# Kernel tuning notes

Measured on AMD Instinct MI355X. Metric: run time of the kernel, lower is better.

## Reference

```python
import jax, jax.numpy as jnp
import numpy as np

NUM_EXPERTS = 4
TOP_K = 2


def setup_inputs() -> dict:
    key = jax.random.key(0)
    ks = jax.random.split(key, 16)
    B, L, D, E, H = 8, 768, 1024, NUM_EXPERTS, 4096
    s = 0.02
    return {
        "context_c": jax.random.normal(ks[0], (B, L, D), jnp.float32),
        "time_cond": jax.random.normal(ks[1], (B, D), jnp.float32),
        "gate_w": jax.random.normal(ks[2], (3 * D, E), jnp.float32) * s,
        "gate_b": jnp.zeros((E,), jnp.float32),
        "time_w": jax.random.normal(ks[3], (D, 2 * E), jnp.float32) * s,
        "time_b": jnp.zeros((2 * E,), jnp.float32),
        "ew1": jax.random.normal(ks[4], (E, D, H), jnp.float32) * s,
        "eb1": jnp.zeros((E, H), jnp.float32),
        "ew2": jax.random.normal(ks[5], (E, H, D), jnp.float32) * s,
        "eb2": jnp.zeros((E, D), jnp.float32),
        "sw1": jax.random.normal(ks[6], (D, H), jnp.float32) * s,
        "sb1": jnp.zeros((H,), jnp.float32),
        "sw2": jax.random.normal(ks[7], (H, D), jnp.float32) * s,
        "sb2": jnp.zeros((D,), jnp.float32),
    }


def reference(context_c, time_cond, gate_w, gate_b, time_w, time_b,
              ew1, eb1, ew2, eb2, sw1, sb1, sw2, sb2):
    B, L, D = context_c.shape
    E, K = NUM_EXPERTS, TOP_K
    L_head = L_wrist = L // 3

    head = context_c[:, :L_head]                       # (B, Lh, D)
    wrist = context_c[:, L_head:L_head + L_wrist]      # (B, Lw, D)
    proprio = context_c[:, L_head + L_wrist:]          # (B, Lp, D)

    # modality-combination aggregates for the gate
    full_agg = context_c.mean(axis=1)
    hp_agg = jnp.concatenate([head, proprio], axis=1).mean(axis=1)
    wp_agg = jnp.concatenate([wrist, proprio], axis=1).mean(axis=1)
    gate_in = jnp.concatenate([full_agg, hp_agg, wp_agg], axis=-1)  # (B, 3D)

    gate_logits = gate_in @ gate_w + gate_b            # (B, E)
    mod = jax.nn.silu(time_cond) @ time_w + time_b     # (B, 2E)
    scale, shift = jnp.split(mod, 2, axis=-1)
    gate_logits = gate_logits * (1.0 + scale) + shift

    gate_scores = jax.nn.softmax(gate_logits, axis=-1)
    topk_w, topk_i = jax.lax.top_k(gate_scores, K)     # (B, K)
    topk_w = topk_w / (topk_w.sum(axis=-1, keepdims=True) + 1e-8)

    # per-sample combine weight per expert: (B, E)
    onehot = (topk_i[..., None] == jnp.arange(E)[None, None, :]).astype(context_c.dtype)
    w_be = jnp.sum(topk_w[..., None] * onehot, axis=1)

    # modality token masks per expert: expert 1 skips wrist, expert 2 skips head
    mask = np.ones((E, L), dtype=np.float32)
    mask[1, L_head:L_head + L_wrist] = 0.0
    mask[2, :L_head] = 0.0
    mask = jnp.asarray(mask)

    out = jnp.zeros_like(context_c)
    for e in range(E):  # small fixed expert loop; FFN is tokenwise so masking == routing
        h = jax.nn.gelu(context_c @ ew1[e] + eb1[e], approximate=True)
        y = h @ ew2[e] + eb2[e]                        # (B, L, D)
        out = out + (w_be[:, e][:, None, None] * mask[e][None, :, None]) * y

    shared = jax.nn.gelu(context_c @ sw1 + sb1, approximate=True) @ sw2 + sb2
    return out + shared
```

## Files before the change

### kernel.cpp

```cpp
#include <hip/hip_runtime.h>

using bf16x8 = __attribute__((ext_vector_type(8))) short;
using f32x4  = __attribute__((ext_vector_type(4))) float;
using u16x4  = __attribute__((ext_vector_type(4))) unsigned short;

#define AS1(p) ((__attribute__((address_space(1))) void*)(p))
#define AS3(p) ((__attribute__((address_space(3))) void*)(p))

__device__ __forceinline__ unsigned short f2bf(float f){
  unsigned int x = __float_as_uint(f);
  unsigned int r = (x + 0x7FFFu + ((x >> 16) & 1u)) >> 16;
  return (unsigned short)r;
}
__device__ __forceinline__ float gelu_tanh(float x){
  float u = 0.7978845608028654f * (x + 0.044715f * x * x * x);
  float t = 1.f - 2.f / (__expf(2.f * u) + 1.f);
  return 0.5f * x * (1.f + t);
}

static constexpr int BB = 8, LL = 768, DD = 1024, HH = 4096, TT = 6144;

__global__ __launch_bounds__(256) void k0_transpose(const float* __restrict__ srcE,
                                                    const float* __restrict__ srcS,
                                                    unsigned short* __restrict__ dst,
                                                    int R, int C){
  __shared__ float tile[64][65];
  int z = blockIdx.z;
  const float* src = (z < 4) ? srcE + (size_t)z * R * C : srcS;
  unsigned short* d = dst + (size_t)z * R * C;
  int c0 = blockIdx.x * 64, r0 = blockIdx.y * 64;
  int tx = threadIdx.x & 15, ty = threadIdx.x >> 4;
  #pragma unroll
  for (int rep = 0; rep < 4; rep++){
    int r = ty + rep * 16;
    float4 v = *(const float4*)(src + (size_t)(r0 + r) * C + c0 + tx * 4);
    tile[r][tx * 4 + 0] = v.x; tile[r][tx * 4 + 1] = v.y;
    tile[r][tx * 4 + 2] = v.z; tile[r][tx * 4 + 3] = v.w;
  }
  __syncthreads();
  #pragma unroll
  for (int rep = 0; rep < 4; rep++){
    int c = ty + rep * 16;
    u16x4 o;
    o[0] = f2bf(tile[tx * 4 + 0][c]); o[1] = f2bf(tile[tx * 4 + 1][c]);
    o[2] = f2bf(tile[tx * 4 + 2][c]); o[3] = f2bf(tile[tx * 4 + 3][c]);
    *(u16x4*)(d + (size_t)(c0 + c) * R + r0 + tx * 4) = o;
  }
}

__global__ __launch_bounds__(256) void k1x_cvt_partial(const float* __restrict__ X,
                                                       unsigned short* __restrict__ Xb,
                                                       float* __restrict__ part){
  int ch = blockIdx.x, b = blockIdx.y, t = threadIdx.x;
  size_t rowbase = ((size_t)(b * LL + ch * 32)) * DD;
  const float4* src = (const float4*)(X + rowbase);
  u16x4* dst = (u16x4*)(Xb + rowbase);
  float4 s; s.x = s.y = s.z = s.w = 0.f;
  for (int l = 0; l < 32; l++){
    float4 v = src[l * 256 + t];
    u16x4 o;
    o[0] = f2bf(v.x); o[1] = f2bf(v.y); o[2] = f2bf(v.z); o[3] = f2bf(v.w);
    dst[l * 256 + t] = o;
    s.x += v.x; s.y += v.y; s.z += v.z; s.w += v.w;
  }
  ((float4*)(part + ((size_t)(b * 24 + ch)) * DD))[t] = s;
}

__global__ __launch_bounds__(256) void k1b_gate(const float* __restrict__ part,
                                                const float* __restrict__ tc,
                                                const float* __restrict__ gw,
                                                const float* __restrict__ gb,
                                                const float* __restrict__ tw,
                                                const float* __restrict__ tb,
                                                float* __restrict__ wtop, int* __restrict__ itop){
  int b = blockIdx.x, t = threadIdx.x;
  __shared__ float glog[4], gmod[8];
  if (t < 4) glog[t] = 0.f;
  if (t < 8) gmod[t] = 0.f;
  __syncthreads();
  float lacc[4] = {0.f,0.f,0.f,0.f};
  float macc[8] = {0.f,0.f,0.f,0.f,0.f,0.f,0.f,0.f};
  for (int dd = 0; dd < 4; dd++){
    int d = dd * 256 + t;
    const float* pb = part + (size_t)b * 24 * DD + d;
    float sh = 0.f, sw = 0.f, sp = 0.f;
    for (int c2 = 0; c2 < 8; c2++){
      sh += pb[(0  + c2) * DD];
      sw += pb[(8  + c2) * DD];
      sp += pb[(16 + c2) * DD];
    }
    float fa = (sh + sw + sp) * (1.f / 768.f);
    float hp = (sh + sp) * (1.f / 512.f);
    float wp = (sw + sp) * (1.f / 512.f);
    #pragma unroll
    for (int e = 0; e < 4; e++){
      lacc[e] += fa * gw[(size_t)d * 4 + e]
               + hp * gw[(size_t)(DD + d) * 4 + e]
               + wp * gw[(size_t)(2 * DD + d) * 4 + e];
    }
    float v = tc[(size_t)b * DD + d];
    float sl = v / (1.f + __expf(-v));
    #pragma unroll
    for (int j = 0; j < 8; j++) macc[j] += sl * tw[(size_t)d * 8 + j];
  }
  #pragma unroll
  for (int e = 0; e < 4; e++) atomicAdd(&glog[e], lacc[e]);
  #pragma unroll
  for (int j = 0; j < 8; j++) atomicAdd(&gmod[j], macc[j]);
  __syncthreads();
  if (t == 0){
    float lg[4];
    #pragma unroll
    for (int e = 0; e < 4; e++){
      float sc = gmod[e]     + tb[e];
      float sf = gmod[4 + e] + tb[4 + e];
      lg[e] = (glog[e] + gb[e]) * (1.f + sc) + sf;
    }
    float mx = fmaxf(fmaxf(lg[0], lg[1]), fmaxf(lg[2], lg[3]));
    float p[4], s = 0.f;
    #pragma unroll
    for (int e = 0; e < 4; e++){ p[e] = __expf(lg[e] - mx); s += p[e]; }
    #pragma unroll
    for (int e = 0; e < 4; e++) p[e] /= s;
    int i0 = 0;
    for (int e = 1; e < 4; e++) if (p[e] > p[i0]) i0 = e;
    int i1 = (i0 == 0) ? 1 : 0;
    for (int e = 0; e < 4; e++) if (e != i0 && p[e] > p[i1]) i1 = e;
    float den = p[i0] + p[i1] + 1e-8f;
    wtop[b * 2 + 0] = p[i0] / den;  wtop[b * 2 + 1] = p[i1] / den;
    itop[b * 2 + 0] = i0;           itop[b * 2 + 1] = i1;
  }
}

__device__ __forceinline__ void gemm_core(const unsigned short* __restrict__ A,
                                          const unsigned short* __restrict__ B,
                                          size_t lda, size_t ldb, int nkt,
                                          unsigned short* ldsA, unsigned short* ldsB,
                                          f32x4 (&acc)[4][4]){
  int tid = threadIdx.x;
  int lane = tid & 63, wave = tid >> 6;
  int quad = lane >> 4, r = lane & 15;
  int wm = (wave >> 1) * 64, wn = (wave & 1) * 64;
  int wavebase = tid & 192;
  for (int kt = 0; kt < nkt; kt++){
    int k0 = kt * 64;
    #pragma unroll
    for (int i = 0; i < 4; i++){
      int g = i * 256 + tid;
      int m = g >> 3, slot = g & 7;
      int c = slot ^ (m & 7);
      const unsigned short* gpA = A + (size_t)m * lda + (k0 + c * 8);
      const unsigned short* gpB = B + (size_t)m * ldb + (k0 + c * 8);
      unsigned short* lp = ldsA + (size_t)(i * 256 + wavebase) * 8;
      __builtin_amdgcn_global_load_lds(AS1(gpA), AS3(lp), 16, 0, 0);
      unsigned short* lq = ldsB + (size_t)(i * 256 + wavebase) * 8;
      __builtin_amdgcn_global_load_lds(AS1(gpB), AS3(lq), 16, 0, 0);
    }
    __syncthreads();
    #pragma unroll
    for (int ks = 0; ks < 2; ks++){
      int cc = ks * 4 + quad;
      bf16x8 af[4], bfv[4];
      #pragma unroll
      for (int t2 = 0; t2 < 4; t2++){
        int m = wm + t2 * 16 + r;
        af[t2] = *(const bf16x8*)(ldsA + ((size_t)m * 8 + (cc ^ (m & 7))) * 8);
        int n = wn + t2 * 16 + r;
        bfv[t2] = *(const bf16x8*)(ldsB + ((size_t)n * 8 + (cc ^ (n & 7))) * 8);
      }
      #pragma unroll
      for (int mi = 0; mi < 4; mi++)
        #pragma unroll
        for (int ni = 0; ni < 4; ni++)
          acc[mi][ni] = __builtin_amdgcn_mfma_f32_16x16x32_bf16(af[mi], bfv[ni], acc[mi][ni], 0, 0, 0);
    }
    __syncthreads();
  }
}

__device__ __forceinline__ void mask_weight(int e, int seg, float& w){
  if ((e == 1 && seg == 1) || (e == 2 && seg == 0)) w = 0.f;
}

__global__ __launch_bounds__(256) void k2_gemm1(const unsigned short* __restrict__ Xb,
                                                const unsigned short* __restrict__ w1t,
                                                const float* __restrict__ eb1,
                                                const float* __restrict__ sb1,
                                                const float* __restrict__ wtop,
                                                const int* __restrict__ itop,
                                                unsigned short* __restrict__ Hws){
  int m0 = blockIdx.x * 128, n0 = blockIdx.y * 128, slot = blockIdx.z;
  int b = m0 / LL, seg = (m0 % LL) / 256;
  int mat; float w;
  if (slot == 0){ mat = 4; w = 1.f; }
  else {
    int k = slot - 1;
    mat = itop[b * 2 + k];
    w = wtop[b * 2 + k];
    mask_weight(mat, seg, w);
    if (w == 0.f) return;
  }
  __shared__ __align__(16) unsigned short ldsA[128 * 64];
  __shared__ __align__(16) unsigned short ldsB[128 * 64];
  f32x4 acc[4][4];
  #pragma unroll
  for (int mi = 0; mi < 4; mi++)
    #pragma unroll
    for (int ni = 0; ni < 4; ni++)
      #pragma unroll
      for (int c = 0; c < 4; c++) acc[mi][ni][c] = 0.f;

  const unsigned short* Abase = Xb + (size_t)m0 * DD;
  const unsigned short* Bbase = w1t + (size_t)mat * HH * DD + (size_t)n0 * DD;
  gemm_core(Abase, Bbase, DD, DD, DD / 64, ldsA, ldsB, acc);

  int tid = threadIdx.x, lane = tid & 63, wave = tid >> 6;
  int quad = lane >> 4, r = lane & 15;
  int wm = (wave >> 1) * 64, wn = (wave & 1) * 64;
  const float* b1 = (mat == 4) ? sb1 : eb1 + (size_t)mat * HH;
  unsigned short* Hout = Hws + (size_t)slot * TT * HH;
  #pragma unroll
  for (int ni = 0; ni < 4; ni++){
    int col = n0 + wn + ni * 16 + r;
    float bias = b1[col];
    #pragma unroll
    for (int mi = 0; mi < 4; mi++){
      #pragma unroll
      for (int r2 = 0; r2 < 4; r2++){
        int row = m0 + wm + mi * 16 + quad * 4 + r2;
        float v = gelu_tanh(acc[mi][ni][r2] + bias) * w;
        Hout[(size_t)row * HH + col] = f2bf(v);
      }
    }
  }
}

__global__ __launch_bounds__(256) void k3a_gemm2(const unsigned short* __restrict__ Hws,
                                                 const unsigned short* __restrict__ w2t,
                                                 const float* __restrict__ eb2,
                                                 const float* __restrict__ sb2,
                                                 const float* __restrict__ wtop,
                                                 const int* __restrict__ itop,
                                                 float* __restrict__ out,
                                                 float* __restrict__ p1){
  int m0 = blockIdx.x * 128, n0 = blockIdx.y * 128, kh = blockIdx.z;
  int b = m0 / LL, seg = (m0 % LL) / 256;
  __shared__ __align__(16) unsigned short ldsA[128 * 64];
  __shared__ __align__(16) unsigned short ldsB[128 * 64];
  f32x4 acc[4][4];
  #pragma unroll
  for (int mi = 0; mi < 4; mi++)
    #pragma unroll
    for (int ni = 0; ni < 4; ni++)
      #pragma unroll
      for (int c = 0; c < 4; c++) acc[mi][ni][c] = 0.f;

  int emat[2]; float ew[2];
  #pragma unroll
  for (int k = 0; k < 2; k++){
    emat[k] = itop[b * 2 + k];
    ew[k] = wtop[b * 2 + k];
    mask_weight(emat[k], seg, ew[k]);
  }
  for (int slot = 0; slot < 3; slot++){
    int mat;
    if (slot == 0) mat = 4;
    else { if (ew[slot - 1] == 0.f) continue; mat = emat[slot - 1]; }
    const unsigned short* Abase = Hws + (size_t)slot * TT * HH + (size_t)m0 * HH + kh * 2048;
    const unsigned short* Bbase = w2t + (size_t)mat * DD * HH + (size_t)n0 * HH + kh * 2048;
    gemm_core(Abase, Bbase, HH, HH, 2048 / 64, ldsA, ldsB, acc);
  }
  int tid = threadIdx.x, lane = tid & 63, wave = tid >> 6;
  int quad = lane >> 4, r = lane & 15;
  int wm = (wave >> 1) * 64, wn = (wave & 1) * 64;
  if (kh == 0){
    #pragma unroll
    for (int ni = 0; ni < 4; ni++){
      int col = n0 + wn + ni * 16 + r;
      float bias = sb2[col];
      if (ew[0] > 0.f) bias += ew[0] * eb2[(size_t)emat[0] * DD + col];
      if (ew[1] > 0.f) bias += ew[1] * eb2[(size_t)emat[1] * DD + col];
      #pragma unroll
      for (int mi = 0; mi < 4; mi++)
        #pragma unroll
        for (int r2 = 0; r2 < 4; r2++){
          int row = m0 + wm + mi * 16 + quad * 4 + r2;
          out[(size_t)row * DD + col] = acc[mi][ni][r2] + bias;
        }
    }
  } else {
    #pragma unroll
    for (int ni = 0; ni < 4; ni++){
      int col = n0 + wn + ni * 16 + r;
      #pragma unroll
      for (int mi = 0; mi < 4; mi++)
        #pragma unroll
        for (int r2 = 0; r2 < 4; r2++){
          int row = m0 + wm + mi * 16 + quad * 4 + r2;
          p1[(size_t)row * DD + col] = acc[mi][ni][r2];
        }
    }
  }
}

__global__ __launch_bounds__(256) void k3r_reduce(float* __restrict__ out,
                                                  const float* __restrict__ p1){
  size_t i = (size_t)blockIdx.x * 256 + threadIdx.x;
  float4 a = ((const float4*)out)[i];
  float4 b = ((const float4*)p1)[i];
  a.x += b.x; a.y += b.y; a.z += b.z; a.w += b.w;
  ((float4*)out)[i] = a;
}

extern "C" void kernel_launch(void* const* d_in, const int* in_sizes, int n_in,
                              void* d_out, int out_size, void* d_ws, size_t ws_size,
                              hipStream_t stream){
  const float* X   = (const float*)d_in[0];
  const float* tc  = (const float*)d_in[1];
  const float* gw  = (const float*)d_in[2];
  const float* gb  = (const float*)d_in[3];
  const float* tw  = (const float*)d_in[4];
  const float* tb  = (const float*)d_in[5];
  const float* ew1 = (const float*)d_in[6];
  const float* eb1 = (const float*)d_in[7];
  const float* ew2 = (const float*)d_in[8];
  const float* eb2 = (const float*)d_in[9];
  const float* sw1 = (const float*)d_in[10];
  const float* sb1 = (const float*)d_in[11];
  const float* sw2 = (const float*)d_in[12];
  const float* sb2 = (const float*)d_in[13];
  float* out = (float*)d_out;
  char* ws = (char*)d_ws;

  const size_t off_part = 0;
  const size_t off_wtop = 786432;
  const size_t off_itop = 786560;
  const size_t off_xb   = 1ull << 20;
  const size_t off_w1t  = 14ull << 20;
  const size_t off_w2t  = off_w1t + 41943040ull;
  const size_t off_h    = off_w2t + 41943040ull;
  const size_t need     = off_h + 150994944ull;
  if (ws_size < need) return;

  float* part = (float*)(ws + off_part);
  float* wtop = (float*)(ws + off_wtop);
  int*   itop = (int*)(ws + off_itop);
  unsigned short* Xb  = (unsigned short*)(ws + off_xb);
  unsigned short* w1t = (unsigned short*)(ws + off_w1t);
  unsigned short* w2t = (unsigned short*)(ws + off_w2t);
  unsigned short* Hws = (unsigned short*)(ws + off_h);
  float* p1 = (float*)(ws + off_w1t);

  k1x_cvt_partial<<<dim3(24, 8), 256, 0, stream>>>(X, Xb, part);
  k0_transpose<<<dim3(64, 16, 5), 256, 0, stream>>>(ew1, sw1, w1t, 1024, 4096);
  k0_transpose<<<dim3(16, 64, 5), 256, 0, stream>>>(ew2, sw2, w2t, 4096, 1024);
  k1b_gate<<<dim3(8), 256, 0, stream>>>(part, tc, gw, gb, tw, tb, wtop, itop);
  k2_gemm1<<<dim3(48, 32, 3), 256, 0, stream>>>(Xb, w1t, eb1, sb1, wtop, itop, Hws);
  k3a_gemm2<<<dim3(48, 8, 2), 256, 0, stream>>>(Hws, w2t, eb2, sb2, wtop, itop, out, p1);
  k3r_reduce<<<dim3(6144), 256, 0, stream>>>(out, p1);
}
```

Baseline: 712.2 us.

## Switch GEMMs to 256x256 tiles with 8 waves and double-buffered LDS pipeline

Replaces the 128x128, 4-wave GEMM core with a 256x256 tile computed by 8 waves. LDS is double-buffered, and global-to-LDS prefetches for later K steps are interleaved between quarter-tile MFMA phases, using explicit barriers, waitcnt and setprio. The goal is more data reuse per byte loaded and hiding global load latency behind MFMA work. The cost is a much larger LDS footprint (128KB per block) and fewer blocks in the k3a_gemm2 grid (192 instead of 768), which may underfill the GPU.

```diff
diff --git a/kernel.cpp b/kernel.cpp
--- a/kernel.cpp
+++ b/kernel.cpp
@@ -132,49 +132,117 @@
   }
 }
 
-__device__ __forceinline__ void gemm_core(const unsigned short* __restrict__ A,
-                                          const unsigned short* __restrict__ B,
-                                          size_t lda, size_t ldb, int nkt,
-                                          unsigned short* ldsA, unsigned short* ldsB,
-                                          f32x4 (&acc)[4][4]){
-  int tid = threadIdx.x;
-  int lane = tid & 63, wave = tid >> 6;
-  int quad = lane >> 4, r = lane & 15;
-  int wm = (wave >> 1) * 64, wn = (wave & 1) * 64;
-  int wavebase = tid & 192;
+#define MMA_Q(AF, BQ, MH, NH)                                                   \
+  {                                                                             \
+    _Pragma("unroll") for (int ks = 0; ks < 2; ks++)                            \
+    _Pragma("unroll") for (int mf = 0; mf < 4; mf++)                            \
+    _Pragma("unroll") for (int nf = 0; nf < 2; nf++)                            \
+      acc[(MH)*4+mf][(NH)*2+nf] = __builtin_amdgcn_mfma_f32_16x16x32_bf16(      \
+          (AF)[mf][ks], (BQ)[nf][ks], acc[(MH)*4+mf][(NH)*2+nf], 0, 0, 0);      \
+  }
+
+__device__ __forceinline__ void gemm256_core(const unsigned short* __restrict__ A,
+                                             const unsigned short* __restrict__ B,
+                                             int lda, int ldb, int nkt,
+                                             unsigned short* ldsA,
+                                             unsigned short* ldsB,
+                                             f32x4 (&acc)[8][4]){
+  const int t = threadIdx.x;
+  const int lane = t & 63, quad = lane >> 4, r = lane & 15;
+  const int wave = t >> 6, wm = wave >> 2, wn = wave & 3;
+  const int welem = (t & 448) * 8;
+
+  int offA[2], offB[2];
+  #pragma unroll
+  for (int j = 0; j < 2; j++){
+    int x = t * 16 + j * 8192;
+    int y = x ^ (((x >> 9) & 1) << 5);
+    int cr = y >> 7, kel = (y & 127) >> 1;
+    offA[j] = (((cr >> 6) << 7) + (cr & 63)) * lda + kel;
+    offB[j] = (((cr >> 5) << 6) + (cr & 31)) * ldb + kel;
+  }
+  const int ldam = 64 * lda, ldbn = 32 * ldb;
+
+  auto stA = [&](int buf, int mh, int kt){
+    #pragma unroll
+    for (int j = 0; j < 2; j++)
+      __builtin_amdgcn_global_load_lds(AS1(A + offA[j] + mh * ldam + kt * 64),
+          AS3(ldsA + (buf * 2 + mh) * 8192 + welem + j * 4096), 16, 0, 0);
+  };
+  auto stB = [&](int buf, int nh, int kt){
+    #pragma unroll
+    for (int j = 0; j < 2; j++)
+      __builtin_amdgcn_global_load_lds(AS1(B + offB[j] + nh * ldbn + kt * 64),
+          AS3(ldsB + (buf * 2 + nh) * 8192 + welem + j * 4096), 16, 0, 0);
+  };
+  auto ldA = [&](int buf, int mh, bf16x8 (&dst)[4][2]){
+    #pragma unroll
+    for (int mf = 0; mf < 4; mf++){
+      int cr = wm * 64 + mf * 16 + r;
+      const unsigned short* p = ldsA + (buf * 2 + mh) * 8192 + cr * 64;
+      int sw = (cr & 4) ? 16 : 0;
+      dst[mf][0] = *(const bf16x8*)(p + ((quad * 8) ^ sw));
+      dst[mf][1] = *(const bf16x8*)(p + 32 + ((quad * 8) ^ sw));
+    }
+  };
+  auto ldB = [&](int buf, int nh, bf16x8 (&dst)[2][2]){
+    #pragma unroll
+    for (int nf = 0; nf < 2; nf++){
+      int cc = wn * 32 + nf * 16 + r;
+      const unsigned short* p = ldsB + (buf * 2 + nh) * 8192 + cc * 64;
+      int sw = (cc & 4) ? 16 : 0;
+      dst[nf][0] = *(const bf16x8*)(p + ((quad * 8) ^ sw));
+      dst[nf][1] = *(const bf16x8*)(p + 32 + ((quad * 8) ^ sw));
+    }
+  };
+
+  stA(0, 0, 0); stB(0, 0, 0); stB(0, 1, 0); stA(0, 1, 0);
+  stA(1, 0, 1); stB(1, 0, 1); stB(1, 1, 1);
+  asm volatile("s_waitcnt vmcnt(6)" ::: "memory");
+  __builtin_amdgcn_s_barrier();
+
+  bf16x8 af[4][2], b0[2][2], b1[2][2];
   for (int kt = 0; kt < nkt; kt++){
-    int k0 = kt * 64;
-    #pragma unroll
-    for (int i = 0; i < 4; i++){
-      int g = i * 256 + tid;
-      int m = g >> 3, slot = g & 7;
-      int c = slot ^ (m & 7);
-      const unsigned short* gpA = A + (size_t)m * lda + (k0 + c * 8);
-      const unsigned short* gpB = B + (size_t)m * ldb + (k0 + c * 8);
-      unsigned short* lp = ldsA + (size_t)(i * 256 + wavebase) * 8;
-      __builtin_amdgcn_global_load_lds(AS1(gpA), AS3(lp), 16, 0, 0);
-      unsigned short* lq = ldsB + (size_t)(i * 256 + wavebase) * 8;
-      __builtin_amdgcn_global_load_lds(AS1(gpB), AS3(lq), 16, 0, 0);
-    }
-    __syncthreads();
-    #pragma unroll
-    for (int ks = 0; ks < 2; ks++){
-      int cc = ks * 4 + quad;
-      bf16x8 af[4], bfv[4];
-      #pragma unroll
-      for (int t2 = 0; t2 < 4; t2++){
-        int m = wm + t2 * 16 + r;
-        af[t2] = *(const bf16x8*)(ldsA + ((size_t)m * 8 + (cc ^ (m & 7))) * 8);
-        int n = wn + t2 * 16 + r;
-        bfv[t2] = *(const bf16x8*)(ldsB + ((size_t)n * 8 + (cc ^ (n & 7))) * 8);
-      }
-      #pragma unroll
-      for (int mi = 0; mi < 4; mi++)
-        #pragma unroll
-        for (int ni = 0; ni < 4; ni++)
-          acc[mi][ni] = __builtin_amdgcn_mfma_f32_16x16x32_bf16(af[mi], bfv[ni], acc[mi][ni], 0, 0, 0);
-    }
-    __syncthreads();
+    int buf = kt & 1;
+    bool pf1 = (kt + 1 < nkt), pf2 = (kt + 2 < nkt);
+    ldA(buf, 0, af); ldB(buf, 0, b0);
+    if (pf1) stA(buf ^ 1, 1, kt + 1);
+    __builtin_amdgcn_s_barrier();
+    asm volatile("s_waitcnt lgkmcnt(0)" ::: "memory");
+    __builtin_amdgcn_sched_barrier(0);
+    __builtin_amdgcn_s_setprio(1);
+    MMA_Q(af, b0, 0, 0);
+    __builtin_amdgcn_s_setprio(0);
+    __builtin_amdgcn_s_barrier();
+    ldB(buf, 1, b1);
+    if (pf2) stA(buf, 0, kt + 2);
+    __builtin_amdgcn_s_barrier();
+    asm volatile("s_waitcnt lgkmcnt(0)" ::: "memory");
+    __builtin_amdgcn_sched_barrier(0);
+    __builtin_amdgcn_s_setprio(1);
+    MMA_Q(af, b1, 0, 1);
+    __builtin_amdgcn_s_setprio(0);
+    __builtin_amdgcn_s_barrier();
+    ldA(buf, 1, af);
+    if (pf2) stB(buf, 0, kt + 2);
+    __builtin_amdgcn_s_barrier();
+    asm volatile("s_waitcnt lgkmcnt(0)" ::: "memory");
+    __builtin_amdgcn_sched_barrier(0);
+    __builtin_amdgcn_s_setprio(1);
+    MMA_Q(af, b1, 1, 1);
+    __builtin_amdgcn_s_setprio(0);
+    __builtin_amdgcn_s_barrier();
+    if (pf2) stB(buf, 1, kt + 2);
+    __builtin_amdgcn_s_barrier();
+    __builtin_amdgcn_sched_barrier(0);
+    __builtin_amdgcn_s_setprio(1);
+    MMA_Q(af, b0, 1, 0);
+    __builtin_amdgcn_s_setprio(0);
+    if (pf1){
+      if (pf2) asm volatile("s_waitcnt vmcnt(6)" ::: "memory");
+      else     asm volatile("s_waitcnt vmcnt(0)" ::: "memory");
+    }
+    __builtin_amdgcn_s_barrier();
   }
 }
 
@@ -182,14 +250,14 @@
   if ((e == 1 && seg == 1) || (e == 2 && seg == 0)) w = 0.f;
 }
 
-__global__ __launch_bounds__(256) void k2_gemm1(const unsigned short* __restrict__ Xb,
-                                                const unsigned short* __restrict__ w1t,
-                                                const float* __restrict__ eb1,
-                                                const float* __restrict__ sb1,
-                                                const float* __restrict__ wtop,
-                                                const int* __restrict__ itop,
-                                                unsigned short* __restrict__ Hws){
-  int m0 = blockIdx.x * 128, n0 = blockIdx.y * 128, slot = blockIdx.z;
+__global__ __launch_bounds__(512, 2) void k2_gemm1(const unsigned short* __restrict__ Xb,
+                                                   const unsigned short* __restrict__ w1t,
+                                                   const float* __restrict__ eb1,
+                                                   const float* __restrict__ sb1,
+                                                   const float* __restrict__ wtop,
+                                                   const int* __restrict__ itop,
+                                                   unsigned short* __restrict__ Hws){
+  int m0 = blockIdx.x * 256, n0 = blockIdx.y * 256, slot = blockIdx.z;
   int b = m0 / LL, seg = (m0 % LL) / 256;
   int mat; float w;
   if (slot == 0){ mat = 4; w = 1.f; }
@@ -200,56 +268,54 @@
     mask_weight(mat, seg, w);
     if (w == 0.f) return;
   }
-  __shared__ __align__(16) unsigned short ldsA[128 * 64];
-  __shared__ __align__(16) unsigned short ldsB[128 * 64];
-  f32x4 acc[4][4];
-  #pragma unroll
-  for (int mi = 0; mi < 4; mi++)
+  __shared__ __align__(16) unsigned short ldsA[32768];
+  __shared__ __align__(16) unsigned short ldsB[32768];
+  f32x4 acc[8][4];
+  #pragma unroll
+  for (int mi = 0; mi < 8; mi++)
     #pragma unroll
     for (int ni = 0; ni < 4; ni++)
       #pragma unroll
       for (int c = 0; c < 4; c++) acc[mi][ni][c] = 0.f;
 
-  const unsigned short* Abase = Xb + (size_t)m0 * DD;
-  const unsigned short* Bbase = w1t + (size_t)mat * HH * DD + (size_t)n0 * DD;
-  gemm_core(Abase, Bbase, DD, DD, DD / 64, ldsA, ldsB, acc);
-
-  int tid = threadIdx.x, lane = tid & 63, wave = tid >> 6;
-  int quad = lane >> 4, r = lane & 15;
-  int wm = (wave >> 1) * 64, wn = (wave & 1) * 64;
+  gemm256_core(Xb + (size_t)m0 * DD,
+               w1t + (size_t)mat * HH * DD + (size_t)n0 * DD,
+               DD, DD, DD / 64, ldsA, ldsB, acc);
+
+  int t = threadIdx.x, lane = t & 63, wave = t >> 6;
+  int quad = lane >> 4, r = lane & 15, wm = wave >> 2, wn = wave & 3;
   const float* b1 = (mat == 4) ? sb1 : eb1 + (size_t)mat * HH;
   unsigned short* Hout = Hws + (size_t)slot * TT * HH;
   #pragma unroll
   for (int ni = 0; ni < 4; ni++){
-    int col = n0 + wn + ni * 16 + r;
+    int col = n0 + wn * 64 + ni * 16 + r;
     float bias = b1[col];
     #pragma unroll
-    for (int mi = 0; mi < 4; mi++){
+    for (int mi = 0; mi < 8; mi++){
       #pragma unroll
       for (int r2 = 0; r2 < 4; r2++){
-        int row = m0 + wm + mi * 16 + quad * 4 + r2;
-        float v = gelu_tanh(acc[mi][ni][r2] + bias) * w;
-        Hout[(size_t)row * HH + col] = f2bf(v);
+        int row = m0 + wm * 128 + mi * 16 + quad * 4 + r2;
+        Hout[(size_t)row * HH + col] = f2bf(gelu_tanh(acc[mi][ni][r2] + bias) * w);
       }
     }
   }
 }
 
-__global__ __launch_bounds__(256) void k3a_gemm2(const unsigned short* __restrict__ Hws,
-                                                 const unsigned short* __restrict__ w2t,
-                                                 const float* __restrict__ eb2,
-                                                 const float* __restrict__ sb2,
-                                                 const float* __restrict__ wtop,
-                                                 const int* __restrict__ itop,
-                                                 float* __restrict__ out,
-                                                 float* __restrict__ p1){
-  int m0 = blockIdx.x * 128, n0 = blockIdx.y * 128, kh = blockIdx.z;
+__global__ __launch_bounds__(512, 2) void k3a_gemm2(const unsigned short* __restrict__ Hws,
+                                                    const unsigned short* __restrict__ w2t,
+                                                    const float* __restrict__ eb2,
+                                                    const float* __restrict__ sb2,
+                                                    const float* __restrict__ wtop,
+                                                    const int* __restrict__ itop,
+                                                    float* __restrict__ out,
+                                                    float* __restrict__ p1){
+  int m0 = blockIdx.x * 256, n0 = blockIdx.y * 256, kh = blockIdx.z;
   int b = m0 / LL, seg = (m0 % LL) / 256;
-  __shared__ __align__(16) unsigned short ldsA[128 * 64];
-  __shared__ __align__(16) unsigned short ldsB[128 * 64];
-  f32x4 acc[4][4];
-  #pragma unroll
-  for (int mi = 0; mi < 4; mi++)
+  __shared__ __align__(16) unsigned short ldsA[32768];
+  __shared__ __align__(16) unsigned short ldsB[32768];
+  f32x4 acc[8][4];
+  #pragma unroll
+  for (int mi = 0; mi < 8; mi++)
     #pragma unroll
     for (int ni = 0; ni < 4; ni++)
       #pragma unroll
@@ -266,37 +332,36 @@
     int mat;
     if (slot == 0) mat = 4;
     else { if (ew[slot - 1] == 0.f) continue; mat = emat[slot - 1]; }
-    const unsigned short* Abase = Hws + (size_t)slot * TT * HH + (size_t)m0 * HH + kh * 2048;
-    const unsigned short* Bbase = w2t + (size_t)mat * DD * HH + (size_t)n0 * HH + kh * 2048;
-    gemm_core(Abase, Bbase, HH, HH, 2048 / 64, ldsA, ldsB, acc);
-  }
-  int tid = threadIdx.x, lane = tid & 63, wave = tid >> 6;
-  int quad = lane >> 4, r = lane & 15;
-  int wm = (wave >> 1) * 64, wn = (wave & 1) * 64;
+    gemm256_core(Hws + (size_t)slot * TT * HH + (size_t)m0 * HH + kh * 2048,
+                 w2t + (size_t)mat * DD * HH + (size_t)n0 * HH + kh * 2048,
+                 HH, HH, 2048 / 64, ldsA, ldsB, acc);
+  }
+  int t = threadIdx.x, lane = t & 63, wave = t >> 6;
+  int quad = lane >> 4, r = lane & 15, wm = wave >> 2, wn = wave & 3;
   if (kh == 0){
     #pragma unroll
     for (int ni = 0; ni < 4; ni++){
-      int col = n0 + wn + ni * 16 + r;
+      int col = n0 + wn * 64 + ni * 16 + r;
       float bias = sb2[col];
       if (ew[0] > 0.f) bias += ew[0] * eb2[(size_t)emat[0] * DD + col];
       if (ew[1] > 0.f) bias += ew[1] * eb2[(size_t)emat[1] * DD + col];
       #pragma unroll
-      for (int mi = 0; mi < 4; mi++)
+      for (int mi = 0; mi < 8; mi++)
         #pragma unroll
         for (int r2 = 0; r2 < 4; r2++){
-          int row = m0 + wm + mi * 16 + quad * 4 + r2;
+          int row = m0 + wm * 128 + mi * 16 + quad * 4 + r2;
           out[(size_t)row * DD + col] = acc[mi][ni][r2] + bias;
         }
     }
   } else {
     #pragma unroll
     for (int ni = 0; ni < 4; ni++){
-      int col = n0 + wn + ni * 16 + r;
+      int col = n0 + wn * 64 + ni * 16 + r;
       #pragma unroll
-      for (int mi = 0; mi < 4; mi++)
+      for (int mi = 0; mi < 8; mi++)
         #pragma unroll
         for (int r2 = 0; r2 < 4; r2++){
-          int row = m0 + wm + mi * 16 + quad * 4 + r2;
+          int row = m0 + wm * 128 + mi * 16 + quad * 4 + r2;
           p1[(size_t)row * DD + col] = acc[mi][ni][r2];
         }
     }
@@ -355,7 +420,7 @@
   k0_transpose<<<dim3(64, 16, 5), 256, 0, stream>>>(ew1, sw1, w1t, 1024, 4096);
   k0_transpose<<<dim3(16, 64, 5), 256, 0, stream>>>(ew2, sw2, w2t, 4096, 1024);
   k1b_gate<<<dim3(8), 256, 0, stream>>>(part, tc, gw, gb, tw, tb, wtop, itop);
-  k2_gemm1<<<dim3(48, 32, 3), 256, 0, stream>>>(Xb, w1t, eb1, sb1, wtop, itop, Hws);
-  k3a_gemm2<<<dim3(48, 8, 2), 256, 0, stream>>>(Hws, w2t, eb2, sb2, wtop, itop, out, p1);
+  k2_gemm1<<<dim3(24, 16, 3), 512, 0, stream>>>(Xb, w1t, eb1, sb1, wtop, itop, Hws);
+  k3a_gemm2<<<dim3(24, 4, 2), 512, 0, stream>>>(Hws, w2t, eb2, sb2, wtop, itop, out, p1);
   k3r_reduce<<<dim3(6144), 256, 0, stream>>>(out, p1);
 }
```

Measured after the change: 671.9 us. -5.7%, faster.
